# Kernel tuning notes

Hardware: AMD Instinct MI355X
Metric: run time of the kernel (lower is better)

The kernel has to match this reference:

```python
import jax, jax.numpy as jnp
import numpy as np

B, S, E = 8, 4096, 8          # batch, seq_len, embed_dim (= n_wires)
NUM_HEADS = 2
SCALE = 1.0 / np.sqrt(E // NUM_HEADS).astype(np.float32)  # 1/sqrt(d_k)


def setup_inputs() -> dict:
    key = jax.random.key(0)
    ks = jax.random.split(key, 10)
    s = 1.0 / np.sqrt(E)
    return {
        "x": jax.random.normal(ks[0], (B, S, E), dtype=jnp.float32),
        "Wq": jax.random.uniform(ks[1], (E, E), jnp.float32, -s, s),
        "bq": jax.random.uniform(ks[2], (E,), jnp.float32, -s, s),
        "Wk": jax.random.uniform(ks[3], (E, E), jnp.float32, -s, s),
        "bk": jax.random.uniform(ks[4], (E,), jnp.float32, -s, s),
        "Wv": jax.random.uniform(ks[5], (E, E), jnp.float32, -s, s),
        "bv": jax.random.uniform(ks[6], (E,), jnp.float32, -s, s),
        "theta": jax.random.normal(ks[7], (E,), dtype=jnp.float32),  # shared RX params (qkqv[0])
        "Wc": jax.random.uniform(ks[8], (E, E), jnp.float32, -s, s),
        "bc": jax.random.uniform(ks[9], (E,), jnp.float32, -s, s),
    }


def _qproj(h, theta):
    # RX(h_i) then RX(theta_i) on |0>, measure PauliZ: <Z_i> = cos(h_i + theta_i)
    return jnp.cos(h + theta)


def reference(x, Wq, bq, Wk, bk, Wv, bv, theta, Wc, bc):
    q = _qproj(x @ Wq.T + bq, theta)   # [B,S,E]
    k = _qproj(x @ Wk.T + bk, theta)
    v = _qproj(x @ Wv.T + bv, theta)
    scores = jnp.einsum('bse,bte->bst', q, k) * SCALE  # [B,S,S]
    attn = jax.nn.softmax(scores, axis=-1)             # dropout is identity in eval
    out = jnp.einsum('bst,bte->bse', attn, v)          # [B,S,E]
    return out @ Wc.T + bc
```

## Files before the change

kernel.cpp:

```cpp
#include <hip/hip_runtime.h>
#include <math.h>

#define E_DIM 8
#define S_DIM 4096
#define B_DIM 8
#define NROWS (B_DIM * S_DIM)
#define TCH 512
#define NCHUNK (S_DIM / TCH)
#define VSTRIDE 516

#define QSCALE 0.72134752044448170f

typedef __attribute__((ext_vector_type(4))) float f4;
typedef __attribute__((ext_vector_type(4))) __fp16 h4;
typedef __attribute__((ext_vector_type(2))) __fp16 h2t;

union HU { uint4 u; __fp16 s[8]; };
union QU { uint2 u; h4 h; };

__device__ inline float fast_exp2(float x) {
#if __has_builtin(__builtin_amdgcn_exp2f)
    return __builtin_amdgcn_exp2f(x);
#else
    return exp2f(x);
#endif
}

__global__ __launch_bounds__(256) void qkv_kernel(
    const float* __restrict__ x,
    const float* __restrict__ Wq, const float* __restrict__ bq,
    const float* __restrict__ Wk, const float* __restrict__ bk,
    const float* __restrict__ Wv, const float* __restrict__ bv,
    const float* __restrict__ theta,
    uint2* __restrict__ Qh, uint4* __restrict__ KVh)
{
    int row = blockIdx.x * blockDim.x + threadIdx.x;
    const float4* x4 = (const float4*)(x + (size_t)row * E_DIM);
    float4 xa = x4[0], xb = x4[1];
    float xr[8] = {xa.x, xa.y, xa.z, xa.w, xb.x, xb.y, xb.z, xb.w};

    float q[8], k[8], v[8];
#pragma unroll
    for (int i = 0; i < 8; ++i) {
        float hq = bq[i], hk = bk[i], hv = bv[i];
#pragma unroll
        for (int j = 0; j < 8; ++j) {
            hq += xr[j] * Wq[i * 8 + j];
            hk += xr[j] * Wk[i * 8 + j];
            hv += xr[j] * Wv[i * 8 + j];
        }
        float th = theta[i];
        q[i] = __cosf(hq + th) * QSCALE;
        k[i] = __cosf(hk + th);
        v[i] = __cosf(hv + th);
    }

    union { uint2 u; __fp16 s[4]; } qp[2];
#pragma unroll
    for (int i = 0; i < 8; ++i) qp[i / 4].s[i % 4] = (__fp16)q[i];
    Qh[(size_t)row * 2 + 0] = qp[0].u;
    Qh[(size_t)row * 2 + 1] = qp[1].u;

    HU kv0, kv1;
#pragma unroll
    for (int i = 0; i < 8; ++i) { kv0.s[i] = (__fp16)k[i]; kv1.s[i] = (__fp16)v[i]; }
    KVh[(size_t)row * 2 + 0] = kv0.u;
    KVh[(size_t)row * 2 + 1] = kv1.u;
}

__global__ __launch_bounds__(256) void attn_mfma(
    const uint2* __restrict__ Qh, const uint4* __restrict__ KVh,
    const float* __restrict__ Wc, const float* __restrict__ bc,
    float* __restrict__ out)
{
    __shared__ __align__(16) __fp16 Kpad[TCH * 16];
    __shared__ __align__(16) __fp16 Vt[16 * VSTRIDE];

    int tid = threadIdx.x;
    int l = tid & 63;
    int wv = tid >> 6;
    int b = blockIdx.x;
    int batch = b >> 6;
    int rbase = b * 64 + wv * 16;

    for (int r = tid; r < TCH; r += 256)
        *((uint4*)(Kpad + r * 16 + 8)) = make_uint4(0, 0, 0, 0);
    {
        uint* z = (uint*)(Vt + 9 * VSTRIDE);
        for (int i = tid; i < 7 * VSTRIDE / 2; i += 256) z[i] = 0;
    }
    for (int i = tid; i < VSTRIDE; i += 256) Vt[8 * VSTRIDE + i] = (__fp16)1.0f;

    QU qu; qu.u = make_uint2(0, 0);
    if ((l >> 4) < 2)
        qu.u = Qh[(size_t)(rbase + (l & 15)) * 2 + (l >> 4)];
    h4 qf = qu.h;

    f4 C = {0.f, 0.f, 0.f, 0.f};

    for (int ch = 0; ch < NCHUNK; ++ch) {
        __syncthreads();
        const uint4* src = KVh + ((size_t)batch * S_DIM + (size_t)ch * TCH) * 2;
        for (int tl = tid; tl < TCH; tl += 256) {
            uint4 kk = src[tl * 2];
            uint4 vvu = src[tl * 2 + 1];
            *((uint4*)(Kpad + tl * 16)) = kk;
            HU vv; vv.u = vvu;
#pragma unroll
            for (int e = 0; e < 8; ++e)
                Vt[e * VSTRIDE + tl] = vv.s[e];
        }
        __syncthreads();

#pragma unroll 4
        for (int s = 0; s < TCH / 16; ++s) {
            int ts = s * 16;
            h4 kf = *((const h4*)(Kpad + ((ts + (l & 15)) << 4) + ((l >> 4) << 2)));
            f4 sc = __builtin_amdgcn_mfma_f32_16x16x16f16(
                kf, qf, (f4){0.f, 0.f, 0.f, 0.f}, 0, 0, 0);
            float e0 = fast_exp2(sc[0]);
            float e1 = fast_exp2(sc[1]);
            float e2 = fast_exp2(sc[2]);
            float e3 = fast_exp2(sc[3]);
            h2t p0 = __builtin_amdgcn_cvt_pkrtz(e0, e1);
            h2t p1 = __builtin_amdgcn_cvt_pkrtz(e2, e3);
            h4 af = __builtin_shufflevector(p0, p1, 0, 1, 2, 3);
            h4 vf = *((const h4*)(Vt + (l & 15) * VSTRIDE + ts + ((l >> 4) << 2)));
            C = __builtin_amdgcn_mfma_f32_16x16x16f16(af, vf, C, 0, 0, 0);
        }
    }
    __syncthreads();

    float o[4];
#pragma unroll
    for (int i = 0; i < 4; ++i) {
        float d = __shfl(C[i], (l & 48) | 8, 64);
        o[i] = C[i] / d;
    }

    float* patch = ((float*)Kpad) + wv * 160;
    if ((l & 15) < 8) {
#pragma unroll
        for (int i = 0; i < 4; ++i)
            patch[(((l >> 4) << 2) + i) * 9 + (l & 15)] = o[i];
    }
    __syncthreads();

    int r2 = l >> 2;
    int ep = (l & 3) * 2;
    float vrow[8];
#pragma unroll
    for (int j = 0; j < 8; ++j) vrow[j] = patch[r2 * 9 + j];
    float o0 = bc[ep], o1 = bc[ep + 1];
#pragma unroll
    for (int j = 0; j < 8; ++j) {
        o0 = __builtin_fmaf(vrow[j], Wc[ep * 8 + j], o0);
        o1 = __builtin_fmaf(vrow[j], Wc[(ep + 1) * 8 + j], o1);
    }
    *((float2*)(out + (size_t)(rbase + r2) * 8 + ep)) = make_float2(o0, o1);
}

extern "C" void kernel_launch(void* const* d_in, const int* in_sizes, int n_in,
                              void* d_out, int out_size, void* d_ws, size_t ws_size,
                              hipStream_t stream) {
    const float* x     = (const float*)d_in[0];
    const float* Wq    = (const float*)d_in[1];
    const float* bq    = (const float*)d_in[2];
    const float* Wk    = (const float*)d_in[3];
    const float* bk    = (const float*)d_in[4];
    const float* Wv    = (const float*)d_in[5];
    const float* bv    = (const float*)d_in[6];
    const float* theta = (const float*)d_in[7];
    const float* Wc    = (const float*)d_in[8];
    const float* bc    = (const float*)d_in[9];
    float* out = (float*)d_out;

    float* ws  = (float*)d_ws;
    uint2* Qh  = (uint2*)ws;
    uint4* KVh = (uint4*)(ws + (size_t)NROWS * 4);

    qkv_kernel<<<NROWS / 256, 256, 0, stream>>>(x, Wq, bq, Wk, bk, Wv, bv, theta, Qh, KVh);

    attn_mfma<<<NROWS / 64, 256, 0, stream>>>(Qh, KVh, Wc, bc, out);
}
```

Baseline: 102.6 us.

## Split attention over key ranges, double query rows per wave, pre-transpose V

The attention kernel now gives each wave 32 query rows instead of 16, which reuses each K/V fragment load across two query tiles. It also splits the key dimension four ways across a second grid axis, writing partial numerators and denominators that a new finalize kernel sums, normalizes and projects through Wc. V is stored pre-transposed by the QKV kernel, so shared-memory staging uses 16-byte vector copies instead of scalar scatters. This adds a third launch plus partial-sum traffic through global memory, in exchange for fewer redundant K/V loads and more parallelism.

Measured after the change: 100.8 us. No clear change (-1.7%).

```diff
diff --git a/kernel.cpp b/kernel.cpp
--- a/kernel.cpp
+++ b/kernel.cpp
@@ -6,16 +6,15 @@
 #define B_DIM 8
 #define NROWS (B_DIM * S_DIM)
 #define TCH 512
-#define NCHUNK (S_DIM / TCH)
-#define VSTRIDE 516
+#define TSPLIT 4
+#define VSTRIDE 520
 
 #define QSCALE 0.72134752044448170f
 
 typedef __attribute__((ext_vector_type(4))) float f4;
 typedef __attribute__((ext_vector_type(4))) __fp16 h4;
-typedef __attribute__((ext_vector_type(2))) __fp16 h2t;
-
-union HU { uint4 u; __fp16 s[8]; };
+typedef __attribute__((ext_vector_type(8))) __fp16 h8;
+
 union QU { uint2 u; h4 h; };
 
 __device__ inline float fast_exp2(float x) {
@@ -32,7 +31,7 @@
     const float* __restrict__ Wk, const float* __restrict__ bk,
     const float* __restrict__ Wv, const float* __restrict__ bv,
     const float* __restrict__ theta,
-    uint2* __restrict__ Qh, uint4* __restrict__ KVh)
+    uint4* __restrict__ Qh, uint4* __restrict__ Kg, __fp16* __restrict__ VTg)
 {
     int row = blockIdx.x * blockDim.x + threadIdx.x;
     const float4* x4 = (const float4*)(x + (size_t)row * E_DIM);
@@ -55,23 +54,23 @@
         v[i] = __cosf(hv + th);
     }
 
-    union { uint2 u; __fp16 s[4]; } qp[2];
-#pragma unroll
-    for (int i = 0; i < 8; ++i) qp[i / 4].s[i % 4] = (__fp16)q[i];
-    Qh[(size_t)row * 2 + 0] = qp[0].u;
-    Qh[(size_t)row * 2 + 1] = qp[1].u;
-
-    HU kv0, kv1;
-#pragma unroll
-    for (int i = 0; i < 8; ++i) { kv0.s[i] = (__fp16)k[i]; kv1.s[i] = (__fp16)v[i]; }
-    KVh[(size_t)row * 2 + 0] = kv0.u;
-    KVh[(size_t)row * 2 + 1] = kv1.u;
+    union { uint4 u; __fp16 s[8]; } qp, kp;
+#pragma unroll
+    for (int i = 0; i < 8; ++i) { qp.s[i] = (__fp16)q[i]; kp.s[i] = (__fp16)k[i]; }
+    Qh[row] = qp.u;
+    Kg[row] = kp.u;
+
+    int batch = row >> 12;
+    int t = row & 4095;
+#pragma unroll
+    for (int e = 0; e < 8; ++e)
+        VTg[((size_t)(batch * 8 + e) << 12) + t] = (__fp16)v[e];
 }
 
 __global__ __launch_bounds__(256) void attn_mfma(
-    const uint2* __restrict__ Qh, const uint4* __restrict__ KVh,
-    const float* __restrict__ Wc, const float* __restrict__ bc,
-    float* __restrict__ out)
+    const uint4* __restrict__ Qh, const uint4* __restrict__ Kg,
+    const __fp16* __restrict__ VTg,
+    float* __restrict__ ACC, float* __restrict__ DEN)
 {
     __shared__ __align__(16) __fp16 Kpad[TCH * 16];
     __shared__ __align__(16) __fp16 Vt[16 * VSTRIDE];
@@ -79,85 +78,126 @@
     int tid = threadIdx.x;
     int l = tid & 63;
     int wv = tid >> 6;
-    int b = blockIdx.x;
-    int batch = b >> 6;
-    int rbase = b * 64 + wv * 16;
+    int rb = blockIdx.x;
+    int sp = blockIdx.y;
+    int batch = rb >> 5;
+    int rbase = rb * 128 + wv * 32;
 
     for (int r = tid; r < TCH; r += 256)
         *((uint4*)(Kpad + r * 16 + 8)) = make_uint4(0, 0, 0, 0);
     {
         uint* z = (uint*)(Vt + 9 * VSTRIDE);
         for (int i = tid; i < 7 * VSTRIDE / 2; i += 256) z[i] = 0;
-    }
-    for (int i = tid; i < VSTRIDE; i += 256) Vt[8 * VSTRIDE + i] = (__fp16)1.0f;
-
-    QU qu; qu.u = make_uint2(0, 0);
-    if ((l >> 4) < 2)
-        qu.u = Qh[(size_t)(rbase + (l & 15)) * 2 + (l >> 4)];
-    h4 qf = qu.h;
-
-    f4 C = {0.f, 0.f, 0.f, 0.f};
-
-    for (int ch = 0; ch < NCHUNK; ++ch) {
+        uint* o1 = (uint*)(Vt + 8 * VSTRIDE);
+        for (int i = tid; i < VSTRIDE / 2; i += 256) o1[i] = 0x3C003C00u;
+    }
+
+    QU q0u, q1u; q0u.u = make_uint2(0, 0); q1u.u = make_uint2(0, 0);
+    if ((l >> 4) < 2) {
+        const uint2* Q2 = (const uint2*)Qh;
+        q0u.u = Q2[(size_t)(rbase + (l & 15)) * 2 + (l >> 4)];
+        q1u.u = Q2[(size_t)(rbase + 16 + (l & 15)) * 2 + (l >> 4)];
+    }
+    h4 qf0 = q0u.h, qf1 = q1u.h;
+
+    int koff = ((l & 12) << 1) + (l & 3);
+    int voff = (l & 15) * VSTRIDE + ((l >> 4) << 3);
+
+    f4 C0 = {0.f, 0.f, 0.f, 0.f};
+    f4 C1 = {0.f, 0.f, 0.f, 0.f};
+
+    for (int ch = 0; ch < 1024 / TCH; ++ch) {
+        int tb = sp * 1024 + ch * TCH;
         __syncthreads();
-        const uint4* src = KVh + ((size_t)batch * S_DIM + (size_t)ch * TCH) * 2;
-        for (int tl = tid; tl < TCH; tl += 256) {
-            uint4 kk = src[tl * 2];
-            uint4 vvu = src[tl * 2 + 1];
-            *((uint4*)(Kpad + tl * 16)) = kk;
-            HU vv; vv.u = vvu;
-#pragma unroll
-            for (int e = 0; e < 8; ++e)
-                Vt[e * VSTRIDE + tl] = vv.s[e];
+        {
+            const uint4* src = Kg + ((size_t)batch << 12) + tb;
+            for (int i = tid; i < TCH; i += 256)
+                *((uint4*)(Kpad + i * 16)) = src[i];
+        }
+        {
+            for (int i = tid; i < 8 * (TCH / 8); i += 256) {
+                int e = i >> 6, c = i & 63;
+                const uint4* src = (const uint4*)(VTg + (((size_t)(batch * 8 + e)) << 12) + tb);
+                *((uint4*)(Vt + e * VSTRIDE + c * 8)) = src[c];
+            }
         }
         __syncthreads();
 
 #pragma unroll 4
-        for (int s = 0; s < TCH / 16; ++s) {
-            int ts = s * 16;
-            h4 kf = *((const h4*)(Kpad + ((ts + (l & 15)) << 4) + ((l >> 4) << 2)));
-            f4 sc = __builtin_amdgcn_mfma_f32_16x16x16f16(
-                kf, qf, (f4){0.f, 0.f, 0.f, 0.f}, 0, 0, 0);
-            float e0 = fast_exp2(sc[0]);
-            float e1 = fast_exp2(sc[1]);
-            float e2 = fast_exp2(sc[2]);
-            float e3 = fast_exp2(sc[3]);
-            h2t p0 = __builtin_amdgcn_cvt_pkrtz(e0, e1);
-            h2t p1 = __builtin_amdgcn_cvt_pkrtz(e2, e3);
-            h4 af = __builtin_shufflevector(p0, p1, 0, 1, 2, 3);
-            h4 vf = *((const h4*)(Vt + (l & 15) * VSTRIDE + ts + ((l >> 4) << 2)));
-            C = __builtin_amdgcn_mfma_f32_16x16x16f16(af, vf, C, 0, 0, 0);
-        }
-    }
-    __syncthreads();
-
-    float o[4];
+        for (int ds = 0; ds < TCH / 32; ++ds) {
+            int krow = ds * 32 + koff;
+            h4 kf0 = *((const h4*)(Kpad + (krow << 4) + ((l >> 4) << 2)));
+            h4 kf1 = *((const h4*)(Kpad + ((krow + 4) << 4) + ((l >> 4) << 2)));
+            h8 vr = *((const h8*)(Vt + voff + ds * 32));
+            h4 vlo = __builtin_shufflevector(vr, vr, 0, 1, 2, 3);
+            h4 vhi = __builtin_shufflevector(vr, vr, 4, 5, 6, 7);
+
+            f4 z = {0.f, 0.f, 0.f, 0.f};
+            f4 s00 = __builtin_amdgcn_mfma_f32_16x16x16f16(kf0, qf0, z, 0, 0, 0);
+            f4 s01 = __builtin_amdgcn_mfma_f32_16x16x16f16(kf1, qf0, z, 0, 0, 0);
+            f4 s10 = __builtin_amdgcn_mfma_f32_16x16x16f16(kf0, qf1, z, 0, 0, 0);
+            f4 s11 = __builtin_amdgcn_mfma_f32_16x16x16f16(kf1, qf1, z, 0, 0, 0);
+
+            h4 p00, p01, p10, p11;
+#pragma unroll
+            for (int i = 0; i < 4; ++i) {
+                p00[i] = (__fp16)fast_exp2(s00[i]);
+                p01[i] = (__fp16)fast_exp2(s01[i]);
+                p10[i] = (__fp16)fast_exp2(s10[i]);
+                p11[i] = (__fp16)fast_exp2(s11[i]);
+            }
+            C0 = __builtin_amdgcn_mfma_f32_16x16x16f16(p00, vlo, C0, 0, 0, 0);
+            C0 = __builtin_amdgcn_mfma_f32_16x16x16f16(p01, vhi, C0, 0, 0, 0);
+            C1 = __builtin_amdgcn_mfma_f32_16x16x16f16(p10, vlo, C1, 0, 0, 0);
+            C1 = __builtin_amdgcn_mfma_f32_16x16x16f16(p11, vhi, C1, 0, 0, 0);
+        }
+    }
+
+    int e = l & 15;
+    int g = l >> 4;
 #pragma unroll
     for (int i = 0; i < 4; ++i) {
-        float d = __shfl(C[i], (l & 48) | 8, 64);
-        o[i] = C[i] / d;
-    }
-
-    float* patch = ((float*)Kpad) + wv * 160;
-    if ((l & 15) < 8) {
-#pragma unroll
-        for (int i = 0; i < 4; ++i)
-            patch[(((l >> 4) << 2) + i) * 9 + (l & 15)] = o[i];
-    }
-    __syncthreads();
-
-    int r2 = l >> 2;
-    int ep = (l & 3) * 2;
-    float vrow[8];
-#pragma unroll
-    for (int j = 0; j < 8; ++j) vrow[j] = patch[r2 * 9 + j];
-    float o0 = bc[ep], o1 = bc[ep + 1];
-#pragma unroll
-    for (int j = 0; j < 8; ++j) {
-        o0 = __builtin_fmaf(vrow[j], Wc[ep * 8 + j], o0);
-        o1 = __builtin_fmaf(vrow[j], Wc[(ep + 1) * 8 + j], o1);
-    }
-    *((float2*)(out + (size_t)(rbase + r2) * 8 + ep)) = make_float2(o0, o1);
+        int r0 = rbase + 4 * g + i;
+        if (e < 8) {
+            ACC[(((size_t)sp * NROWS + r0) << 3) + e] = C0[i];
+            ACC[(((size_t)sp * NROWS + r0 + 16) << 3) + e] = C1[i];
+        } else if (e == 8) {
+            DEN[(size_t)sp * NROWS + r0] = C0[i];
+            DEN[(size_t)sp * NROWS + r0 + 16] = C1[i];
+        }
+    }
+}
+
+__global__ __launch_bounds__(256) void finalize_kernel(
+    const float* __restrict__ ACC, const float* __restrict__ DEN,
+    const float* __restrict__ Wc, const float* __restrict__ bc,
+    float* __restrict__ out)
+{
+    int row = blockIdx.x * blockDim.x + threadIdx.x;
+    float a[8] = {0,0,0,0,0,0,0,0};
+    float den = 0.f;
+#pragma unroll
+    for (int sp = 0; sp < TSPLIT; ++sp) {
+        const float4* A4 = (const float4*)(ACC + (((size_t)sp * NROWS + row) << 3));
+        float4 p0 = A4[0], p1 = A4[1];
+        a[0] += p0.x; a[1] += p0.y; a[2] += p0.z; a[3] += p0.w;
+        a[4] += p1.x; a[5] += p1.y; a[6] += p1.z; a[7] += p1.w;
+        den += DEN[(size_t)sp * NROWS + row];
+    }
+    float inv = 1.0f / den;
+#pragma unroll
+    for (int j = 0; j < 8; ++j) a[j] *= inv;
+    float r[8];
+#pragma unroll
+    for (int i = 0; i < 8; ++i) {
+        float h = bc[i];
+#pragma unroll
+        for (int j = 0; j < 8; ++j) h += a[j] * Wc[i * 8 + j];
+        r[i] = h;
+    }
+    float4* O4 = (float4*)(out + (size_t)row * 8);
+    O4[0] = make_float4(r[0], r[1], r[2], r[3]);
+    O4[1] = make_float4(r[4], r[5], r[6], r[7]);
 }
 
 extern "C" void kernel_launch(void* const* d_in, const int* in_sizes, int n_in,
@@ -176,10 +216,16 @@
     float* out = (float*)d_out;
 
     float* ws  = (float*)d_ws;
-    uint2* Qh  = (uint2*)ws;
-    uint4* KVh = (uint4*)(ws + (size_t)NROWS * 4);
-
-    qkv_kernel<<<NROWS / 256, 256, 0, stream>>>(x, Wq, bq, Wk, bk, Wv, bv, theta, Qh, KVh);
-
-    attn_mfma<<<NROWS / 64, 256, 0, stream>>>(Qh, KVh, Wc, bc, out);
-}
+    uint4*  Qh  = (uint4*)ws;
+    uint4*  Kg  = (uint4*)(ws + (size_t)NROWS * 4);
+    __fp16* VTg = (__fp16*)(ws + (size_t)NROWS * 8);
+    float*  ACC = ws + (size_t)NROWS * 12;
+    float*  DEN = ACC + (size_t)TSPLIT * NROWS * 8;
+
+    qkv_kernel<<<NROWS / 256, 256, 0, stream>>>(x, Wq, bq, Wk, bk, Wv, bv, theta, Qh, Kg, VTg);
+
+    dim3 grid2(NROWS / 128, TSPLIT);
+    attn_mfma<<<grid2, 256, 0, stream>>>(Qh, Kg, VTg, ACC, DEN);
+
+    finalize_kernel<<<NROWS / 256, 256, 0, stream>>>(ACC, DEN, Wc, bc, out);
+}
```
